# Performance work log

Measured on AMD Instinct MI355X. Metric: run time of the kernel, lower is better.

Reference implementation:

```python
import jax, jax.numpy as jnp
import numpy as np

N = 50000        # nodes
E = 800000       # random edges (plus N self-loops added in setup)
DIN = 128        # input_dim
H = 128          # hidden_dim
L = 3            # num_layers
EPS = 1e-5       # BatchNorm1d eps


def _bn(x, gamma, beta):
    # BatchNorm1d in training mode: batch stats over node axis, biased variance
    m = x.mean(axis=0)
    v = jnp.mean((x - m) ** 2, axis=0)
    return (x - m) * jax.lax.rsqrt(v + EPS) * gamma + beta


def setup_inputs() -> dict:
    key = jax.random.key(0)
    ks = jax.random.split(key, 11)
    feats = jax.random.normal(ks[0], (N, DIN), dtype=jnp.float32)
    # edge list with self-loops so every node has degree >= 1 (average pooling divides by degree)
    loops = jnp.arange(N, dtype=jnp.int64)
    src = jnp.concatenate([jax.random.randint(ks[1], (E,), 0, N, dtype=jnp.int64), loops])
    dst = jnp.concatenate([jax.random.randint(ks[2], (E,), 0, N, dtype=jnp.int64), loops])
    s = 0.05
    # per-layer MLP params (num_mlp_layers=2: Linear -> BN -> ReLU -> Linear), layer 0 has DIN==H
    W1 = jax.random.normal(ks[3], (L, DIN, H), dtype=jnp.float32) * s
    b1 = jnp.zeros((L, H), jnp.float32)
    g1 = jnp.ones((L, H), jnp.float32)
    be1 = jnp.zeros((L, H), jnp.float32)
    W2 = jax.random.normal(ks[4], (L, H, H), dtype=jnp.float32) * s
    b2 = jnp.zeros((L, H), jnp.float32)
    # outer BatchNorm1d per GNN layer
    og = jnp.ones((L, H), jnp.float32)
    ob = jnp.zeros((L, H), jnp.float32)
    return {"feats": feats, "W1": W1, "b1": b1, "g1": g1, "be1": be1,
            "W2": W2, "b2": b2, "og": og, "ob": ob, "src": src, "dst": dst}


def reference(feats, W1, b1, g1, be1, W2, b2, og, ob, src, dst):
    n = feats.shape[0]
    # degree = spmm(Adj, ones) -- constant across layers
    deg = jax.ops.segment_sum(jnp.ones(src.shape, jnp.float32), dst, num_segments=n)[:, None]
    h = feats
    for l in range(L):
        # pooled = spmm(Adj, h) via edge gather + segment reduce, then 'average' normalize
        pooled = jax.ops.segment_sum(h[src], dst, num_segments=n) / deg
        # GIN-style 2-layer MLP: Linear -> BN -> ReLU -> Linear
        z = jax.nn.relu(_bn(pooled @ W1[l] + b1[l], g1[l], be1[l]))
        z = z @ W2[l] + b2[l]
        # outer BatchNorm + ReLU
        h = jax.nn.relu(_bn(z, og[l], ob[l]))
    return h
```

## Files before the change

### kernel.cpp

```cpp
#include <hip/hip_runtime.h>
#include <hip/hip_bf16.h>
#include <stdint.h>

typedef __hip_bfloat16 bf16;
typedef short bf16x8 __attribute__((ext_vector_type(8)));
typedef float f32x4 __attribute__((ext_vector_type(4)));

#define HF 128
#define EPS 1e-5f
#define BSH 9
#define BROWS 512
#define ECHUNK 8192

static __device__ __forceinline__ uint32_t pack_bf16(float a, float b) {
    union { bf16 h; unsigned short u; } ca, cb;
    ca.h = __float2bfloat16(a);
    cb.h = __float2bfloat16(b);
    return (uint32_t)ca.u | ((uint32_t)cb.u << 16);
}


__global__ __launch_bounds__(256) void k_bcount(const int* __restrict__ dst,
                                                int* __restrict__ bcnt, int ne, int nb) {
    __shared__ int h[128];
    const int tid = threadIdx.x;
    if (tid < nb) h[tid] = 0;
    __syncthreads();
    const int beg = blockIdx.x * ECHUNK;
    const int end = min(beg + ECHUNK, ne);
    for (int i = beg + tid; i < end; i += 256)
        atomicAdd(&h[dst[i] >> BSH], 1);
    __syncthreads();
    if (tid < nb && h[tid]) atomicAdd(&bcnt[tid], h[tid]);
}

__global__ __launch_bounds__(128) void k_bscan(const int* __restrict__ bcnt,
                                               int* __restrict__ bstart,
                                               int* __restrict__ gcursor,
                                               int* __restrict__ rowptr,
                                               int nb, int n, int ne) {
    if (threadIdx.x == 0) {
        int acc = 0;
        for (int b = 0; b < nb; b++) {
            bstart[b] = acc;
            gcursor[b] = acc;
            acc += bcnt[b];
        }
        bstart[nb] = acc;
        rowptr[n] = ne;
    }
}

__global__ __launch_bounds__(256) void k_bscatter(const int* __restrict__ src,
                                                  const int* __restrict__ dst,
                                                  int* __restrict__ gcursor,
                                                  int2* __restrict__ staging, int ne, int nb) {
    __shared__ int h[128], gb[128];
    const int tid = threadIdx.x;
    if (tid < nb) h[tid] = 0;
    __syncthreads();
    const int beg = blockIdx.x * ECHUNK;
    const int end = min(beg + ECHUNK, ne);
    for (int i = beg + tid; i < end; i += 256)
        atomicAdd(&h[dst[i] >> BSH], 1);
    __syncthreads();
    if (tid < nb) {
        int c = h[tid];
        gb[tid] = c ? atomicAdd(&gcursor[tid], c) : 0;
        h[tid] = 0;
    }
    __syncthreads();
    for (int i = beg + tid; i < end; i += 256) {
        int d = dst[i];
        int b = d >> BSH;
        int r = atomicAdd(&h[b], 1);
        staging[(size_t)gb[b] + r] = make_int2(src[i], d);
    }
}

__global__ __launch_bounds__(256) void k_bbuild(const int2* __restrict__ staging,
                                                const int* __restrict__ bstart,
                                                int* __restrict__ rowptr,
                                                float* __restrict__ deginv,
                                                int* __restrict__ csrsrc, int n) {
    __shared__ int hist[BROWS];
    __shared__ int scan[BROWS];
    const int b = blockIdx.x;
    const int tid = threadIdx.x;
    const int rb = b << BSH;
    const int nrows = min(BROWS, n - rb);
    const int ebeg = bstart[b], eend = bstart[b + 1];
    hist[tid] = 0; hist[tid + 256] = 0;
    __syncthreads();
    for (int i = ebeg + tid; i < eend; i += 256)
        atomicAdd(&hist[staging[i].y - rb], 1);
    __syncthreads();
    const int i0 = tid, i1 = tid + 256;
    scan[i0] = hist[i0]; scan[i1] = hist[i1];
    __syncthreads();
    for (int off = 1; off < BROWS; off <<= 1) {
        int v0 = (i0 >= off) ? scan[i0 - off] : 0;
        int v1 = (i1 >= off) ? scan[i1 - off] : 0;
        __syncthreads();
        scan[i0] += v0; scan[i1] += v1;
        __syncthreads();
    }
    for (int r = tid; r < BROWS; r += 256) {
        int c = hist[r];
        int excl = scan[r] - c;
        if (r < nrows) {
            rowptr[rb + r] = ebeg + excl;
            deginv[rb + r] = c ? 1.0f / (float)c : 0.f;
        }
        scan[r] = excl;
    }
    __syncthreads();
    for (int i = ebeg + tid; i < eend; i += 256) {
        int2 e = staging[i];
        int pos = atomicAdd(&scan[e.y - rb], 1);
        csrsrc[ebeg + pos] = e.x;
    }
}

__global__ __launch_bounds__(256) void k_cvt(const float* __restrict__ in,
                                             uint32_t* __restrict__ out, long tot2) {
    long i = (long)blockIdx.x * 256 + threadIdx.x;
    if (i >= tot2) return;
    float2 v = ((const float2*)in)[i];
    out[i] = pack_bf16(v.x, v.y);
}

template <int AFF>
__global__ __launch_bounds__(256) void k_spmm(const uint32_t* __restrict__ hp,
                                              const int* __restrict__ rowptr,
                                              const int* __restrict__ csrsrc,
                                              const float* __restrict__ deginv,
                                              const float* __restrict__ st,
                                              const float* __restrict__ g,
                                              const float* __restrict__ be,
                                              float inv_n,
                                              uint32_t* __restrict__ pooled, int n, int np) {
    const int wid  = (int)((blockIdx.x * 256u + threadIdx.x) >> 6);
    const int lane = threadIdx.x & 63;
    if (wid >= np) return;
    uint32_t* outp = pooled + (size_t)wid * 64 + lane;
    if (wid >= n) { *outp = 0u; return; }
    float sx = 1.f, cx = 0.f, sy = 1.f, cy = 0.f;
    if (AFF) {
        const int c0 = lane * 2, c1 = c0 + 1;
        float m0 = st[c0] * inv_n, v0 = st[128 + c0] * inv_n - m0 * m0;
        sx = g[c0] * rsqrtf(v0 + EPS); cx = be[c0] - m0 * sx;
        float m1 = st[c1] * inv_n, v1 = st[128 + c1] * inv_n - m1 * m1;
        sy = g[c1] * rsqrtf(v1 + EPS); cy = be[c1] - m1 * sy;
    }
    float a0 = 0.f, a1 = 0.f;
    const int beg = rowptr[wid], end = rowptr[wid + 1];
    for (int base = beg; base < end; base += 64) {
        const int rem = end - base;
        const int cnt = rem < 64 ? rem : 64;
        const int off = lane < cnt ? lane : cnt - 1;
        const int idx = csrsrc[base + off];
        int j = 0;
        for (; j + 8 <= cnt; j += 8) {
            uint32_t p[8];
#pragma unroll
            for (int u = 0; u < 8; u++) {
                int s = __builtin_amdgcn_readlane(idx, j + u);
                p[u] = hp[(size_t)s * 64 + lane];
            }
#pragma unroll
            for (int u = 0; u < 8; u++) {
                float vx = __uint_as_float(p[u] << 16);
                float vy = __uint_as_float(p[u] & 0xFFFF0000u);
                if (AFF) {
                    vx = fmaxf(fmaf(vx, sx, cx), 0.f);
                    vy = fmaxf(fmaf(vy, sy, cy), 0.f);
                }
                a0 += vx; a1 += vy;
            }
        }
        for (; j < cnt; j++) {
            int s = __builtin_amdgcn_readlane(idx, j);
            uint32_t pk = hp[(size_t)s * 64 + lane];
            float vx = __uint_as_float(pk << 16);
            float vy = __uint_as_float(pk & 0xFFFF0000u);
            if (AFF) {
                vx = fmaxf(fmaf(vx, sx, cx), 0.f);
                vy = fmaxf(fmaf(vy, sy, cy), 0.f);
            }
            a0 += vx; a1 += vy;
        }
    }
    const float di = deginv[wid];
    *outp = pack_bf16(a0 * di, a1 * di);
}

template <int MODE, int OUTBF>
__global__ __launch_bounds__(256) void k_gemm(const bf16* __restrict__ Abf,
                                              const float* __restrict__ Af,
                                              const float* __restrict__ W,
                                              const float* __restrict__ bias,
                                              const float* __restrict__ st,
                                              const float* __restrict__ g,
                                              const float* __restrict__ be,
                                              float inv_n,
                                              float* __restrict__ Yf,
                                              bf16* __restrict__ Yb,
                                              float* __restrict__ outstats, int n) {
    __shared__ bf16 WTh[128 * 136];
    __shared__ bf16 WTl[128 * 136];
    __shared__ float sred[4][128];
    __shared__ float sred2[4][128];
    __shared__ float aff[256];
    const int tid = threadIdx.x;
    if (MODE == 1 && tid < 128) {
        float m = st[tid] * inv_n;
        float v = st[128 + tid] * inv_n - m * m;
        float a = g[tid] * rsqrtf(v + EPS);
        aff[tid] = a;
        aff[128 + tid] = be[tid] - m * a;
    }
    for (int idx = tid; idx < 128 * 128; idx += 256) {
        int k = idx >> 7, nn = idx & 127;
        float w = W[idx];
        bf16 h = __float2bfloat16(w);
        WTh[nn * 136 + k] = h;
        WTl[nn * 136 + k] = __float2bfloat16(w - __bfloat162float(h));
    }
    __syncthreads();

    const int wave = tid >> 6, lane = tid & 63;
    const int lrow = lane & 15, quad = lane >> 4;
    const int bx = (int)blockIdx.x * 128;
    int mb[2];
    mb[0] = bx + wave * 16;
    mb[1] = bx + 64 + wave * 16;

    bf16x8 ah[2][4], al[2][4];
#pragma unroll
    for (int rt = 0; rt < 2; rt++) {
        if (MODE == 0) {
            const bf16* arow = Abf + (size_t)(mb[rt] + lrow) * 128 + quad * 8;
#pragma unroll
            for (int kt = 0; kt < 4; kt++)
                ah[rt][kt] = *(const bf16x8*)(arow + kt * 32);
        } else {
            const float* arow = Af + (size_t)(mb[rt] + lrow) * 128 + quad * 8;
#pragma unroll
            for (int kt = 0; kt < 4; kt++) {
                short th[8], tl[8];
#pragma unroll
                for (int j = 0; j < 8; j++) {
                    int k = kt * 32 + quad * 8 + j;
                    float x = fmaxf(fmaf(arow[kt * 32 + j], aff[k], aff[128 + k]), 0.f);
                    union { bf16 b; short s; } ch, cl;
                    ch.b = __float2bfloat16(x);
                    cl.b = __float2bfloat16(x - __bfloat162float(ch.b));
                    th[j] = ch.s; tl[j] = cl.s;
                }
                ah[rt][kt] = *(bf16x8*)th;
                al[rt][kt] = *(bf16x8*)tl;
            }
        }
    }

    f32x4 acc[2][8];
#pragma unroll
    for (int rt = 0; rt < 2; rt++)
#pragma unroll
        for (int nt = 0; nt < 8; nt++) acc[rt][nt] = (f32x4){0.f, 0.f, 0.f, 0.f};

#pragma unroll
    for (int nt = 0; nt < 8; nt++) {
        const bf16* wh = &WTh[(nt * 16 + lrow) * 136 + quad * 8];
        const bf16* wl = &WTl[(nt * 16 + lrow) * 136 + quad * 8];
#pragma unroll
        for (int kt = 0; kt < 4; kt++) {
            bf16x8 bh = *(const bf16x8*)(wh + kt * 32);
            bf16x8 bl = *(const bf16x8*)(wl + kt * 32);
#pragma unroll
            for (int rt = 0; rt < 2; rt++) {
                acc[rt][nt] = __builtin_amdgcn_mfma_f32_16x16x32_bf16(ah[rt][kt], bh, acc[rt][nt], 0, 0, 0);
                acc[rt][nt] = __builtin_amdgcn_mfma_f32_16x16x32_bf16(ah[rt][kt], bl, acc[rt][nt], 0, 0, 0);
                if (MODE == 1)
                    acc[rt][nt] = __builtin_amdgcn_mfma_f32_16x16x32_bf16(al[rt][kt], bh, acc[rt][nt], 0, 0, 0);
            }
        }
    }

#pragma unroll
    for (int nt = 0; nt < 8; nt++) {
        int col = nt * 16 + lrow;
        float bv = bias[col];
        float csum = 0.f, csq = 0.f;
#pragma unroll
        for (int rt = 0; rt < 2; rt++) {
#pragma unroll
            for (int r = 0; r < 4; r++) {
                int row = mb[rt] + quad * 4 + r;
                float yv = acc[rt][nt][r] + bv;
                if (OUTBF) Yb[(size_t)row * 128 + col] = __float2bfloat16(yv);
                else       Yf[(size_t)row * 128 + col] = yv;
                if (row < n) { csum += yv; csq += yv * yv; }
            }
        }
        csum += __shfl_xor(csum, 16, 64); csum += __shfl_xor(csum, 32, 64);
        csq  += __shfl_xor(csq,  16, 64); csq  += __shfl_xor(csq,  32, 64);
        if (quad == 0) { sred[wave][col] = csum; sred2[wave][col] = csq; }
    }
    __syncthreads();
    if (tid < 128) {
        float s = sred[0][tid] + sred[1][tid] + sred[2][tid] + sred[3][tid];
        float q = sred2[0][tid] + sred2[1][tid] + sred2[2][tid] + sred2[3][tid];
        atomicAdd(&outstats[tid], s);
        atomicAdd(&outstats[128 + tid], q);
    }
}

__global__ __launch_bounds__(256) void k_bnrelu(const uint32_t* __restrict__ Z,
                                                const float* __restrict__ st,
                                                const float* __restrict__ g,
                                                const float* __restrict__ be,
                                                float inv_n,
                                                float* __restrict__ out, long tot2) {
    long i = (long)blockIdx.x * 256 + threadIdx.x;
    if (i >= tot2) return;
    int c = (int)((i * 2) & 127);
    float m0 = st[c] * inv_n,     v0 = st[128 + c] * inv_n - m0 * m0;
    float a0 = g[c] * rsqrtf(v0 + EPS),     c0 = be[c] - m0 * a0;
    float m1 = st[c + 1] * inv_n, v1 = st[129 + c] * inv_n - m1 * m1;
    float a1 = g[c + 1] * rsqrtf(v1 + EPS), c1 = be[c + 1] - m1 * a1;
    uint32_t pk = Z[i];
    float vx = __uint_as_float(pk << 16);
    float vy = __uint_as_float(pk & 0xFFFF0000u);
    float2 o;
    o.x = fmaxf(fmaf(vx, a0, c0), 0.f);
    o.y = fmaxf(fmaf(vy, a1, c1), 0.f);
    ((float2*)out)[i] = o;
}

extern "C" void kernel_launch(void* const* d_in, const int* in_sizes, int n_in,
                              void* d_out, int out_size, void* d_ws, size_t ws_size,
                              hipStream_t stream) {
    const float* feats = (const float*)d_in[0];
    const float* W1    = (const float*)d_in[1];
    const float* b1    = (const float*)d_in[2];
    const float* g1    = (const float*)d_in[3];
    const float* be1   = (const float*)d_in[4];
    const float* W2    = (const float*)d_in[5];
    const float* b2    = (const float*)d_in[6];
    const float* og    = (const float*)d_in[7];
    const float* ob    = (const float*)d_in[8];
    const int*   src   = (const int*)d_in[9];
    const int*   dst   = (const int*)d_in[10];

    const int n  = in_sizes[0] / HF;
    const int ne = in_sizes[9];
    const int np = (n + 127) & ~127;
    const int nb = (n + BROWS - 1) >> BSH;

    char* p = (char*)d_ws;
    auto alloc = [&](size_t bytes) -> char* {
        char* r = p;
        p += (bytes + 511) & ~(size_t)511;
        return r;
    };
    uint32_t* hbuf    = (uint32_t*)alloc((size_t)np * 64 * 4);
    uint32_t* pooled  = (uint32_t*)alloc((size_t)np * 64 * 4);
    float*    ybuf    = (float*)   alloc((size_t)np * HF * 4);
    uint32_t* zb      = (uint32_t*)alloc((size_t)np * 64 * 4);
    float*    deginv  = (float*)   alloc((size_t)n * 4);
    int*      rowptr  = (int*)     alloc((size_t)(n + 1) * 4);
    int*      csrsrc  = (int*)     alloc((size_t)ne * 4);
    int2*     staging = (int2*)    alloc((size_t)ne * 8);
    int*      bstart  = (int*)     alloc((size_t)(nb + 1) * 4);
    int*      gcursor = (int*)     alloc((size_t)nb * 4);
    char*     zone    = alloc(512 + 6 * 256 * 4);
    int*      bcnt    = (int*)zone;
    float*    stats6  = (float*)(zone + 512);

    hipMemsetAsync(zone, 0, 512 + 6 * 256 * 4, stream);

    const int ebk = (ne + ECHUNK - 1) / ECHUNK;
    k_bcount  <<<ebk, 256, 0, stream>>>(dst, bcnt, ne, nb);
    k_bscan   <<<1, 128, 0, stream>>>(bcnt, bstart, gcursor, rowptr, nb, n, ne);
    k_bscatter<<<ebk, 256, 0, stream>>>(src, dst, gcursor, staging, ne, nb);
    k_bbuild  <<<nb, 256, 0, stream>>>(staging, bstart, rowptr, deginv, csrsrc, n);

    const long tot2  = (long)n * (HF / 2);
    const int bnb    = (int)((tot2 + 255) / 256);
    const int spmmb  = np / 4;
    const int gemmb  = np / 128;
    const float inv_n = 1.0f / (float)n;

    k_cvt<<<bnb, 256, 0, stream>>>(feats, hbuf, tot2);

    for (int l = 0; l < 3; l++) {
        float* sY = stats6 + (2 * l) * 256;
        float* sZ = stats6 + (2 * l + 1) * 256;
        if (l == 0)
            k_spmm<0><<<spmmb, 256, 0, stream>>>(hbuf, rowptr, csrsrc, deginv,
                                                 nullptr, nullptr, nullptr, inv_n,
                                                 pooled, n, np);
        else
            k_spmm<1><<<spmmb, 256, 0, stream>>>(zb, rowptr, csrsrc, deginv,
                                                 stats6 + (2 * (l - 1) + 1) * 256,
                                                 og + (l - 1) * HF, ob + (l - 1) * HF, inv_n,
                                                 pooled, n, np);
        k_gemm<0, 0><<<gemmb, 256, 0, stream>>>((const bf16*)pooled, nullptr,
                                                W1 + (size_t)l * HF * HF, b1 + l * HF,
                                                nullptr, nullptr, nullptr, inv_n,
                                                ybuf, nullptr, sY, n);
        k_gemm<1, 1><<<gemmb, 256, 0, stream>>>(nullptr, ybuf,
                                                W2 + (size_t)l * HF * HF, b2 + l * HF,
                                                sY, g1 + l * HF, be1 + l * HF, inv_n,
                                                nullptr, (bf16*)zb, sZ, n);
    }
    k_bnrelu<<<bnb, 256, 0, stream>>>(zb, stats6 + 5 * 256, og + 2 * HF, ob + 2 * HF,
                                      inv_n, (float*)d_out, tot2);
}
```

Baseline: 406.1 us.

## Pre-convert weights to swizzled bf16 once and async-load them into LDS

Adds a one-time kernel that transposes all six weight matrices to bf16 in an XOR-swizzled layout. Each GEMM block then copies the prepared weights into LDS with direct global-to-LDS loads instead of converting fp32 weights per block. It also drops the low-order weight correction (WTl) and the MFMAs that used it, which halves weight LDS use and cuts MFMA count. The cost is lower precision, since weights are now single bf16 with no hi/lo split.

```diff
diff --git a/kernel.cpp b/kernel.cpp
--- a/kernel.cpp
+++ b/kernel.cpp
@@ -120,6 +120,19 @@
         int pos = atomicAdd(&scan[e.y - rb], 1);
         csrsrc[ebeg + pos] = e.x;
     }
+}
+
+__global__ __launch_bounds__(256) void k_wprep(const float* __restrict__ W1,
+                                               const float* __restrict__ W2,
+                                               bf16* __restrict__ wp) {
+    const int mat = blockIdx.x >> 6;
+    const int idx = ((blockIdx.x & 63) << 8) + threadIdx.x;
+    const int l = mat >> 1;
+    const float* Wsrc = (mat & 1) ? (W2 + l * 16384) : (W1 + l * 16384);
+    const int nn = idx >> 7, k = idx & 127;
+    float w = Wsrc[k * 128 + nn];
+    int pos = nn * 128 + ((((k >> 3) ^ (nn & 7))) << 3) + (k & 7);
+    wp[mat * 16384 + pos] = __float2bfloat16(w);
 }
 
 __global__ __launch_bounds__(256) void k_cvt(const float* __restrict__ in,
@@ -198,7 +211,7 @@
 template <int MODE, int OUTBF>
 __global__ __launch_bounds__(256) void k_gemm(const bf16* __restrict__ Abf,
                                               const float* __restrict__ Af,
-                                              const float* __restrict__ W,
+                                              const bf16* __restrict__ Wp,
                                               const float* __restrict__ bias,
                                               const float* __restrict__ st,
                                               const float* __restrict__ g,
@@ -207,12 +220,24 @@
                                               float* __restrict__ Yf,
                                               bf16* __restrict__ Yb,
                                               float* __restrict__ outstats, int n) {
-    __shared__ bf16 WTh[128 * 136];
-    __shared__ bf16 WTl[128 * 136];
+    __shared__ __align__(16) bf16 WT[128 * 128];
     __shared__ float sred[4][128];
     __shared__ float sred2[4][128];
     __shared__ float aff[256];
     const int tid = threadIdx.x;
+    const int wave = tid >> 6, lane = tid & 63;
+
+    {
+        const char* gsrc = (const char*)Wp + wave * 1024 + lane * 16;
+        char* ldst = (char*)&WT[0] + wave * 1024;
+#pragma unroll
+        for (int i = 0; i < 8; i++) {
+            __builtin_amdgcn_global_load_lds(
+                (const __attribute__((address_space(1))) uint32_t*)(gsrc + i * 4096),
+                (__attribute__((address_space(3))) uint32_t*)(ldst + i * 4096),
+                16, 0, 0);
+        }
+    }
     if (MODE == 1 && tid < 128) {
         float m = st[tid] * inv_n;
         float v = st[128 + tid] * inv_n - m * m;
@@ -220,16 +245,7 @@
         aff[tid] = a;
         aff[128 + tid] = be[tid] - m * a;
     }
-    for (int idx = tid; idx < 128 * 128; idx += 256) {
-        int k = idx >> 7, nn = idx & 127;
-        float w = W[idx];
-        bf16 h = __float2bfloat16(w);
-        WTh[nn * 136 + k] = h;
-        WTl[nn * 136 + k] = __float2bfloat16(w - __bfloat162float(h));
-    }
-    __syncthreads();
-
-    const int wave = tid >> 6, lane = tid & 63;
+
     const int lrow = lane & 15, quad = lane >> 4;
     const int bx = (int)blockIdx.x * 128;
     int mb[2];
@@ -237,14 +253,21 @@
     mb[1] = bx + 64 + wave * 16;
 
     bf16x8 ah[2][4], al[2][4];
-#pragma unroll
-    for (int rt = 0; rt < 2; rt++) {
-        if (MODE == 0) {
+    if (MODE == 0) {
+#pragma unroll
+        for (int rt = 0; rt < 2; rt++) {
             const bf16* arow = Abf + (size_t)(mb[rt] + lrow) * 128 + quad * 8;
 #pragma unroll
             for (int kt = 0; kt < 4; kt++)
                 ah[rt][kt] = *(const bf16x8*)(arow + kt * 32);
-        } else {
+        }
+    }
+
+    __syncthreads();
+
+    if (MODE == 1) {
+#pragma unroll
+        for (int rt = 0; rt < 2; rt++) {
             const float* arow = Af + (size_t)(mb[rt] + lrow) * 128 + quad * 8;
 #pragma unroll
             for (int kt = 0; kt < 4; kt++) {
@@ -270,18 +293,16 @@
 #pragma unroll
         for (int nt = 0; nt < 8; nt++) acc[rt][nt] = (f32x4){0.f, 0.f, 0.f, 0.f};
 
+    const int sw = lrow & 7;
 #pragma unroll
     for (int nt = 0; nt < 8; nt++) {
-        const bf16* wh = &WTh[(nt * 16 + lrow) * 136 + quad * 8];
-        const bf16* wl = &WTl[(nt * 16 + lrow) * 136 + quad * 8];
+        const bf16* wbase = &WT[(nt * 16 + lrow) * 128];
 #pragma unroll
         for (int kt = 0; kt < 4; kt++) {
-            bf16x8 bh = *(const bf16x8*)(wh + kt * 32);
-            bf16x8 bl = *(const bf16x8*)(wl + kt * 32);
+            bf16x8 bh = *(const bf16x8*)(wbase + (((4 * kt + quad) ^ sw) << 3));
 #pragma unroll
             for (int rt = 0; rt < 2; rt++) {
                 acc[rt][nt] = __builtin_amdgcn_mfma_f32_16x16x32_bf16(ah[rt][kt], bh, acc[rt][nt], 0, 0, 0);
-                acc[rt][nt] = __builtin_amdgcn_mfma_f32_16x16x32_bf16(ah[rt][kt], bl, acc[rt][nt], 0, 0, 0);
                 if (MODE == 1)
                     acc[rt][nt] = __builtin_amdgcn_mfma_f32_16x16x32_bf16(al[rt][kt], bh, acc[rt][nt], 0, 0, 0);
             }
@@ -369,6 +390,7 @@
     uint32_t* pooled  = (uint32_t*)alloc((size_t)np * 64 * 4);
     float*    ybuf    = (float*)   alloc((size_t)np * HF * 4);
     uint32_t* zb      = (uint32_t*)alloc((size_t)np * 64 * 4);
+    bf16*     wprep   = (bf16*)    alloc(6 * 16384 * 2);
     float*    deginv  = (float*)   alloc((size_t)n * 4);
     int*      rowptr  = (int*)     alloc((size_t)(n + 1) * 4);
     int*      csrsrc  = (int*)     alloc((size_t)ne * 4);
@@ -382,6 +404,7 @@
     hipMemsetAsync(zone, 0, 512 + 6 * 256 * 4, stream);
 
     const int ebk = (ne + ECHUNK - 1) / ECHUNK;
+    k_wprep   <<<384, 256, 0, stream>>>(W1, W2, wprep);
     k_bcount  <<<ebk, 256, 0, stream>>>(dst, bcnt, ne, nb);
     k_bscan   <<<1, 128, 0, stream>>>(bcnt, bstart, gcursor, rowptr, nb, n, ne);
     k_bscatter<<<ebk, 256, 0, stream>>>(src, dst, gcursor, staging, ne, nb);
@@ -408,11 +431,13 @@
                                                  og + (l - 1) * HF, ob + (l - 1) * HF, inv_n,
                                                  pooled, n, np);
         k_gemm<0, 0><<<gemmb, 256, 0, stream>>>((const bf16*)pooled, nullptr,
-                                                W1 + (size_t)l * HF * HF, b1 + l * HF,
+                                                wprep + (size_t)(2 * l) * 16384,
+                                                b1 + l * HF,
                                                 nullptr, nullptr, nullptr, inv_n,
                                                 ybuf, nullptr, sY, n);
         k_gemm<1, 1><<<gemmb, 256, 0, stream>>>(nullptr, ybuf,
-                                                W2 + (size_t)l * HF * HF, b2 + l * HF,
+                                                wprep + (size_t)(2 * l + 1) * 16384,
+                                                b2 + l * HF,
                                                 sY, g1 + l * HF, be1 + l * HF, inv_n,
                                                 nullptr, (bf16*)zb, sZ, n);
     }
```

Result: faster. 395.0 us (-2.7%).
